# Performance work log

Measured on AMD Instinct MI355X. Metric: run time of the kernel, lower is better.

## Reference

```python
import jax, jax.numpy as jnp
import numpy as np

B, L, C, D, H, EL, DFF, NC, PH = 32, 512, 64, 512, 8, 3, 2048, 8, 256
DK = D // H


def _ln(x, g, b):
    m = jnp.mean(x, -1, keepdims=True)
    v = jnp.var(x, -1, keepdims=True)
    return (x - m) / jnp.sqrt(v + 1e-5) * g + b


def _projector(x, stats, cw, w1, b1, w2, b2, w3):
    # circular Conv1d over feature axis with seq_len input channels -> 1 channel
    xp = jnp.pad(x, ((0, 0), (0, 0), (1, 1)), mode='wrap')  # [B,L,C+2]
    win = jnp.stack([xp[:, :, :-2], xp[:, :, 1:-1], xp[:, :, 2:]], -1)  # [B,L,C,3]
    y = jnp.einsum('bsck,sk->bc', win, cw)  # [B,C]
    h = jnp.concatenate([y, stats[:, 0, :]], -1)  # [B,2C]
    h = jax.nn.relu(h @ w1.T + b1)
    h = jax.nn.relu(h @ w2.T + b2)
    return h @ w3.T


def setup_inputs() -> dict:
    key = jax.random.key(0)
    ks = jax.random.split(key, 20)
    n = lambda i, shape, s=0.02: jax.random.normal(ks[i], shape, jnp.float32) * s
    return {
        'x_enc': jax.random.normal(ks[0], (B, L, C), jnp.float32),
        'emb_conv_w': n(1, (D, C, 3), 0.05),
        'tau_conv_w': n(2, (L, 3), 0.05),
        'tau_w1': n(3, (PH, 2 * C)), 'tau_b1': jnp.zeros((PH,), jnp.float32),
        'tau_w2': n(4, (PH, PH)), 'tau_b2': jnp.zeros((PH,), jnp.float32),
        'tau_w3': n(5, (1, PH)),
        'delta_conv_w': n(6, (L, 3), 0.05),
        'delta_w1': n(7, (PH, 2 * C)), 'delta_b1': jnp.zeros((PH,), jnp.float32),
        'delta_w2': n(8, (PH, PH)), 'delta_b2': jnp.zeros((PH,), jnp.float32),
        'delta_w3': n(9, (L, PH)),
        'Wq': n(10, (EL, D, D)), 'bq': jnp.zeros((EL, D), jnp.float32),
        'Wk': n(11, (EL, D, D)), 'bk': jnp.zeros((EL, D), jnp.float32),
        'Wv': n(12, (EL, D, D)), 'bv': jnp.zeros((EL, D), jnp.float32),
        'Wo': n(13, (EL, D, D)), 'bo': jnp.zeros((EL, D), jnp.float32),
        'ff_w1': n(14, (EL, DFF, D)), 'ff_b1': jnp.zeros((EL, DFF), jnp.float32),
        'ff_w2': n(15, (EL, D, DFF)), 'ff_b2': jnp.zeros((EL, D), jnp.float32),
        'ln1_g': jnp.ones((EL, D), jnp.float32), 'ln1_b': jnp.zeros((EL, D), jnp.float32),
        'ln2_g': jnp.ones((EL, D), jnp.float32), 'ln2_b': jnp.zeros((EL, D), jnp.float32),
        'norm_g': jnp.ones((D,), jnp.float32), 'norm_b': jnp.zeros((D,), jnp.float32),
        'proj_w': n(16, (NC, D * L), 0.005), 'proj_b': jnp.zeros((NC,), jnp.float32),
    }


def reference(x_enc, emb_conv_w, tau_conv_w, tau_w1, tau_b1, tau_w2, tau_b2, tau_w3,
              delta_conv_w, delta_w1, delta_b1, delta_w2, delta_b2, delta_w3,
              Wq, bq, Wk, bk, Wv, bv, Wo, bo, ff_w1, ff_b1, ff_w2, ff_b2,
              ln1_g, ln1_b, ln2_g, ln2_b, norm_g, norm_b, proj_w, proj_b):
    x_raw = jax.lax.stop_gradient(x_enc)
    mean_enc = jax.lax.stop_gradient(jnp.mean(x_enc, 1, keepdims=True))  # [B,1,C]
    std_enc = jax.lax.stop_gradient(jnp.sqrt(jnp.var(x_enc, axis=1, keepdims=True) + 1e-5))
    tau = jnp.exp(_projector(x_raw, std_enc, tau_conv_w, tau_w1, tau_b1, tau_w2, tau_b2, tau_w3))  # [B,1]
    delta = _projector(x_raw, mean_enc, delta_conv_w, delta_w1, delta_b1, delta_w2, delta_b2, delta_w3)  # [B,L]

    # TokenEmbedding: circular Conv1d (kernel 3, no bias) over time + sinusoidal PE
    xp = jnp.pad(x_enc, ((0, 0), (1, 1), (0, 0)), mode='wrap')
    win = jnp.stack([xp[:, :-2], xp[:, 1:-1], xp[:, 2:]], -1)  # [B,L,C,3]
    x = jnp.einsum('blck,dck->bld', win, emb_conv_w)
    pos = jnp.arange(L, dtype=jnp.float32)[:, None]
    div = jnp.exp(jnp.arange(0, D, 2, dtype=jnp.float32) * (-jnp.log(10000.0) / D))
    pe = jnp.zeros((L, D), jnp.float32).at[:, 0::2].set(jnp.sin(pos * div)).at[:, 1::2].set(jnp.cos(pos * div))
    x = x + pe[None]

    scale = 1.0 / jnp.sqrt(jnp.float32(DK))
    tau4 = tau[:, :, None, None]      # [B,1,1,1]
    delta4 = delta[:, None, None, :]  # [B,1,1,S]
    for i in range(EL):
        q = (x @ Wq[i].T + bq[i]).reshape(B, L, H, DK)
        k = (x @ Wk[i].T + bk[i]).reshape(B, L, H, DK)
        v = (x @ Wv[i].T + bv[i]).reshape(B, L, H, DK)
        scores = jnp.einsum('blhe,bshe->bhls', q, k) * tau4 + delta4  # DSAttention rescale/shift
        A = jax.nn.softmax(scale * scores, axis=-1)
        o = jnp.einsum('bhls,bshd->blhd', A, v).reshape(B, L, D)
        x = x + (o @ Wo[i].T + bo[i])
        x = _ln(x, ln1_g[i], ln1_b[i])
        y = jax.nn.gelu(x @ ff_w1[i].T + ff_b1[i], approximate=False)  # conv1 kernel=1 == linear
        y = y @ ff_w2[i].T + ff_b2[i]
        x = _ln(x + y, ln2_g[i], ln2_b[i])
    x = _ln(x, norm_g, norm_b)
    out = jax.nn.gelu(x, approximate=False).reshape(B, -1)
    return out @ proj_w.T + proj_b
```

## Files before the change

### kernel.cpp

```cpp
#include <hip/hip_runtime.h>
#include <hip/hip_bf16.h>
#include <math.h>

#define B_   32
#define L_   512
#define C_   64
#define D_   512
#define H_   8
#define EL_  3
#define DFF_ 2048
#define NC_  8
#define PH_  256
#define DK_  64
#define NTOK (B_*L_)

typedef unsigned short u16;
typedef unsigned int   u32;
typedef __attribute__((ext_vector_type(4))) float f32x4;
typedef __attribute__((ext_vector_type(8))) short s16x8;

__device__ __forceinline__ u16 f2b(float f){
  u32 u = __float_as_uint(f);
  u32 r = (u + 0x7fffu + ((u >> 16) & 1u)) >> 16;
  return (u16)r;
}
__device__ __forceinline__ float b2f(u16 u){ return __uint_as_float(((u32)u) << 16); }

__device__ __forceinline__ void gload16(const void* g, void* l){
  __builtin_amdgcn_global_load_lds(
      (const __attribute__((address_space(1))) u32*)g,
      (__attribute__((address_space(3))) u32*)l, 16, 0, 0);
}

__device__ __forceinline__ float gelu_exact(float x){
  return 0.5f * x * (1.f + erff(x * 0.70710678118654752f));
}


__global__ __launch_bounds__(256) void k_stats(const float* __restrict__ x,
    float* __restrict__ mean, float* __restrict__ stdv){
  int b = blockIdx.x, t = threadIdx.x;
  const float* p = x + (size_t)b*L_*C_;
  float s = 0.f, q = 0.f;
  for (int i = t; i < L_*C_; i += 256){ float v = p[i]; s += v; q += v*v; }
  __shared__ float ss[256], qq[256];
  ss[t] = s; qq[t] = q;
  __syncthreads();
  if (t < 64){
    float S = ss[t]+ss[t+64]+ss[t+128]+ss[t+192];
    float Q = qq[t]+qq[t+64]+qq[t+128]+qq[t+192];
    float m = S*(1.f/L_);
    mean[b*64+t] = m;
    stdv[b*64+t] = sqrtf(Q*(1.f/L_) - m*m + 1e-5f);
  }
}

__global__ __launch_bounds__(256) void k_mlp(const float* __restrict__ x,
    const float* __restrict__ mean, const float* __restrict__ stdv,
    const float* __restrict__ cw_t, const float* __restrict__ w1t, const float* __restrict__ b1t,
    const float* __restrict__ w2t, const float* __restrict__ b2t, const float* __restrict__ w3t,
    const float* __restrict__ cw_d, const float* __restrict__ w1d, const float* __restrict__ b1d,
    const float* __restrict__ w2d, const float* __restrict__ b2d, const float* __restrict__ w3d,
    float* __restrict__ tau, float* __restrict__ delta)
{
  int b = blockIdx.x, sel = blockIdx.y, t = threadIdx.x;
  const float* cw = sel ? cw_d : cw_t;
  const float* w1 = sel ? w1d : w1t;  const float* b1 = sel ? b1d : b1t;
  const float* w2 = sel ? w2d : w2t;  const float* b2 = sel ? b2d : b2t;
  const float* st = sel ? mean : stdv;
  __shared__ float h0[128], h1s[256], h2s[256], red[256];
  __shared__ float c4[4][64];
  {
    int c = t & 63, g = t >> 6;
    int cm = (c+63)&63, cp = (c+1)&63;
    const float* xrow = x + (size_t)b*L_*C_;
    float acc = 0.f;
    for (int s = g*128; s < (g+1)*128; ++s){
      const float* r = xrow + s*C_;
      acc += r[cm]*cw[s*3] + r[c]*cw[s*3+1] + r[cp]*cw[s*3+2];
    }
    c4[g][c] = acc;
  }
  __syncthreads();
  if (t < 64)       h0[t] = c4[0][t]+c4[1][t]+c4[2][t]+c4[3][t];
  else if (t < 128) h0[t] = st[b*64 + (t-64)];
  __syncthreads();
  { float a = b1[t]; for (int j=0;j<128;++j) a += h0[j]*w1[t*128+j]; h1s[t] = fmaxf(a,0.f); }
  __syncthreads();
  { float a = b2[t]; for (int j=0;j<256;++j) a += h1s[j]*w2[t*256+j]; h2s[t] = fmaxf(a,0.f); }
  __syncthreads();
  if (sel == 0){
    red[t] = h2s[t]*w3t[t];
    __syncthreads();
    for (int o=128;o>0;o>>=1){ if (t<o) red[t]+=red[t+o]; __syncthreads(); }
    if (t == 0) tau[b] = expf(red[0]);
  } else {
    for (int l = t; l < L_; l += 256){
      float a = 0.f;
      for (int j=0;j<256;++j) a += h2s[j]*w3d[l*256+j];
      delta[b*L_ + l] = a;
    }
  }
}

__global__ void k_pe(float* __restrict__ pe){
  int i = blockIdx.x*256 + threadIdx.x;
  if (i >= L_*D_/2) return;
  int l = i >> 8, j = i & 255;
  float div = expf((float)(2*j) * (-9.210340371976184f / (float)D_));
  float arg = (float)l * div;
  pe[l*D_ + 2*j]   = sinf(arg);
  pe[l*D_ + 2*j+1] = cosf(arg);
}

__global__ void k_awin(const float* __restrict__ x, u16* __restrict__ awin){
  int i = blockIdx.x*256 + threadIdx.x;
  if (i >= NTOK*192) return;
  int col = i % 192, row = i / 192;
  int k = col >> 6, c = col & 63;
  int b = row >> 9, l = row & 511;
  int ls = (l + k + 511) & 511;
  awin[i] = f2b(x[((size_t)((b<<9) | ls))*64 + c]);
}

__global__ void k_embw(const float* __restrict__ w, u16* __restrict__ o){
  int i = blockIdx.x*256 + threadIdx.x;
  if (i >= D_*192) return;
  int d = i / 192, col = i % 192, k = col >> 6, c = col & 63;
  o[i] = f2b(w[(d*64 + c)*3 + k]);
}

__global__ void k_packqkv(const float* __restrict__ Wq, const float* __restrict__ Wk,
                          const float* __restrict__ Wv, u16* __restrict__ o){
  int i = blockIdx.x*256 + threadIdx.x;
  if (i >= EL_*1536*D_) return;
  int e = i / (1536*D_), r = i % (1536*D_);
  int n = r / D_, k = r % D_;
  const float* src = (n < 512) ? Wq + ((size_t)e*512 + n)*512 + k
                   : (n < 1024) ? Wk + ((size_t)e*512 + (n-512))*512 + k
                                : Wv + ((size_t)e*512 + (n-1024))*512 + k;
  o[i] = f2b(*src);
}
__global__ void k_packb(const float* __restrict__ bq, const float* __restrict__ bk,
                        const float* __restrict__ bv, float* __restrict__ o){
  int i = blockIdx.x*256 + threadIdx.x;
  if (i >= EL_*1536) return;
  int e = i/1536, n = i%1536;
  o[i] = (n<512) ? bq[e*512+n] : (n<1024) ? bk[e*512+n-512] : bv[e*512+n-1024];
}

__global__ void k_f2b(const float* __restrict__ in, u16* __restrict__ out, int n){
  int i = blockIdx.x*256 + threadIdx.x;
  if (i < n) out[i] = f2b(in[i]);
}

__global__ __launch_bounds__(256,2) void k_gemm(
    const u16* __restrict__ A, const u16* __restrict__ Bm,
    int M, int N, int K,
    const float* __restrict__ bias,
    const float* __restrict__ pe,
    int dogelu,
    float* __restrict__ outF, u16* __restrict__ outB)
{
  __shared__ u16 As[128*64];
  __shared__ u16 Bs[128*64];
  int tid = threadIdx.x;
  int l = tid & 63, w = tid >> 6;
  int wr = w >> 1, wc = w & 1;
  int lo = l & 15, lg = l >> 4;

  int flat = blockIdx.x + gridDim.x*blockIdx.y;
  int nwg  = gridDim.x*gridDim.y;
  int n1   = ((nwg & 7) == 0) ? ((flat & 7)*(nwg >> 3) + (flat >> 3)) : flat;
  int bx   = n1 % gridDim.x, by = n1 / gridDim.x;
  int m0 = by * 128, n0 = bx * 128;

  f32x4 acc[4][4];
  #pragma unroll
  for (int m=0;m<4;++m)
    #pragma unroll
    for (int n=0;n<4;++n) acc[m][n] = (f32x4){0.f,0.f,0.f,0.f};

  int ktn = K >> 6;
  for (int kt = 0; kt < ktn; ++kt){
    #pragma unroll
    for (int i=0;i<4;++i){
      int cA = i*256 + tid;
      int row = cA >> 3, colb = (cA & 7)*8;
      gload16(A  + (size_t)(m0+row)*K + kt*64 + colb, &As[cA*8]);
      gload16(Bm + (size_t)(n0+row)*K + kt*64 + colb, &Bs[cA*8]);
    }
    __syncthreads();
    #pragma unroll
    for (int kk=0;kk<2;++kk){
      int ka = kk*32 + lg*8;
      s16x8 af[4], bfr[4];
      #pragma unroll
      for (int m=0;m<4;++m) af[m]  = *(const s16x8*)&As[(wr*64 + m*16 + lo)*64 + ka];
      #pragma unroll
      for (int n=0;n<4;++n) bfr[n] = *(const s16x8*)&Bs[(wc*64 + n*16 + lo)*64 + ka];
      #pragma unroll
      for (int m=0;m<4;++m)
        #pragma unroll
        for (int n=0;n<4;++n)
          acc[m][n] = __builtin_amdgcn_mfma_f32_16x16x32_bf16(af[m], bfr[n], acc[m][n], 0,0,0);
    }
    __syncthreads();
  }

  #pragma unroll
  for (int m=0;m<4;++m){
    int rbase = m0 + wr*64 + m*16 + lg*4;
    #pragma unroll
    for (int n=0;n<4;++n){
      int col = n0 + wc*64 + n*16 + lo;
      float bv = bias ? bias[col] : 0.f;
      #pragma unroll
      for (int r=0;r<4;++r){
        int row = rbase + r;
        float v = acc[m][n][r] + bv;
        if (pe) v += pe[(size_t)(row & 511)*N + col];
        if (dogelu) v = gelu_exact(v);
        size_t o = (size_t)row*N + col;
        if (outF) outF[o] = v;
        if (outB) outB[o] = f2b(v);
      }
    }
  }
}

__global__ __launch_bounds__(256) void k_vt(const u16* __restrict__ qkv, u16* __restrict__ vT){
  int st = blockIdx.x, h = blockIdx.y, b = blockIdx.z;
  __shared__ u16 tile[64][72];
  int t = threadIdx.x;
  int r = t >> 2, q = t & 3;
  const u16* src = qkv + ((size_t)(b*L_ + st*64 + r))*1536 + 1024 + h*64 + q*16;
  #pragma unroll
  for (int j=0;j<16;++j) tile[r][q*16+j] = src[j];
  __syncthreads();
  u16* dst = vT + (((size_t)(b*H_ + h))*64 + r)*L_ + st*64 + q*16;
  #pragma unroll
  for (int j=0;j<16;++j) dst[j] = tile[q*16+j][r];
}

__global__ __launch_bounds__(256) void k_attn(
    const u16* __restrict__ qkv, const u16* __restrict__ vT,
    const float* __restrict__ tau, const float* __restrict__ delta,
    u16* __restrict__ obf)
{
  __shared__ u16 Ks[2][64*64];
  __shared__ u16 Vs[2][64*64];
  __shared__ u16 plds[4][16*64];
  int id = blockIdx.x;
  int qt = id >> 8, hb = id & 255, h = hb >> 5, b = hb & 31;
  int tid = threadIdx.x, l = tid & 63, w = tid >> 6;
  int lo = l & 15, lg = l >> 4;
  int q0 = qt*64 + w*16;

  const u16* qrow = qkv + ((size_t)(b*L_ + q0 + lo))*1536 + h*64;
  s16x8 qf0 = *(const s16x8*)(qrow + lg*8);
  s16x8 qf1 = *(const s16x8*)(qrow + 32 + lg*8);

  const u16* Kg = qkv + (size_t)b*L_*1536 + 512 + h*64;
  const u16* Vg = vT + ((size_t)(b*H_ + h))*64*L_;

  float taus = tau[b] * 0.125f;
  f32x4 oacc[4];
  #pragma unroll
  for (int n=0;n<4;++n) oacc[n] = (f32x4){0.f,0.f,0.f,0.f};
  float mrow[4] = {-3e38f,-3e38f,-3e38f,-3e38f};
  float lrow[4] = {0.f,0.f,0.f,0.f};
  const float* dptr = delta + b*L_;
  u16* pw = &plds[w][0];

  auto STAGE = [&](int buf, int s0){
    #pragma unroll
    for (int i=0;i<2;++i){
      int c = i*256 + tid;
      int row = c >> 3, sub = (c & 7) ^ (row & 7);
      gload16(Kg + (size_t)(s0 + row)*1536 + sub*8, &Ks[buf][c*8]);
      gload16(Vg + (size_t)row*L_ + s0 + sub*8,     &Vs[buf][c*8]);
    }
  };

  STAGE(0, 0);
  __syncthreads();

  int swz = lo & 7;
  for (int it = 0; it < 8; ++it){
    int s0 = it*64, cur = it & 1;
    if (it < 7) STAGE(cur^1, s0 + 64);
    const u16* Kc = &Ks[cur][0];
    const u16* Vc = &Vs[cur][0];

    f32x4 sacc[4];
    #pragma unroll
    for (int t2=0;t2<4;++t2) sacc[t2] = (f32x4){0.f,0.f,0.f,0.f};
    #pragma unroll
    for (int kk=0;kk<2;++kk){
      #pragma unroll
      for (int t2=0;t2<4;++t2){
        s16x8 kf = *(const s16x8*)&Kc[(t2*16 + lo)*64 + (((kk*4 + lg) ^ swz)*8)];
        sacc[t2] = __builtin_amdgcn_mfma_f32_16x16x32_bf16(kk ? qf1 : qf0, kf, sacc[t2], 0,0,0);
      }
    }

    float p[4][4];
    float rm[4] = {-3e38f,-3e38f,-3e38f,-3e38f};
    #pragma unroll
    for (int t2=0;t2<4;++t2){
      float dl = dptr[s0 + t2*16 + lo] * 0.125f;
      #pragma unroll
      for (int r=0;r<4;++r){
        float sc = taus*sacc[t2][r] + dl;
        p[t2][r] = sc;
        rm[r] = fmaxf(rm[r], sc);
      }
    }
    #pragma unroll
    for (int r=0;r<4;++r){
      #pragma unroll
      for (int off=1; off<16; off<<=1) rm[r] = fmaxf(rm[r], __shfl_xor(rm[r], off));
    }
    float alpha[4];
    #pragma unroll
    for (int r=0;r<4;++r){
      float mn = fmaxf(mrow[r], rm[r]);
      alpha[r] = __expf(mrow[r] - mn);
      mrow[r] = mn;
      float acc = 0.f;
      #pragma unroll
      for (int t2=0;t2<4;++t2){ p[t2][r] = __expf(p[t2][r] - mn); acc += p[t2][r]; }
      #pragma unroll
      for (int off=1; off<16; off<<=1) acc += __shfl_xor(acc, off);
      lrow[r] = lrow[r]*alpha[r] + acc;
    }
    #pragma unroll
    for (int n=0;n<4;++n)
      #pragma unroll
      for (int r=0;r<4;++r) oacc[n][r] *= alpha[r];

    #pragma unroll
    for (int t2=0;t2<4;++t2)
      #pragma unroll
      for (int r=0;r<4;++r){
        int q = lg*4 + r;
        int cb = (t2*2 + (lo>>3)) ^ (q & 7);
        pw[q*64 + cb*8 + (lo & 7)] = f2b(p[t2][r]);
      }
    asm volatile("" ::: "memory");
    #pragma unroll
    for (int kk=0;kk<2;++kk){
      s16x8 pa = *(const s16x8*)&pw[lo*64 + (((kk*4 + lg) ^ swz)*8)];
      #pragma unroll
      for (int n=0;n<4;++n){
        s16x8 vf = *(const s16x8*)&Vc[(n*16 + lo)*64 + (((kk*4 + lg) ^ swz)*8)];
        oacc[n] = __builtin_amdgcn_mfma_f32_16x16x32_bf16(pa, vf, oacc[n], 0,0,0);
      }
    }
    __syncthreads();
  }

  float inv[4];
  #pragma unroll
  for (int r=0;r<4;++r) inv[r] = 1.f / lrow[r];
  #pragma unroll
  for (int n=0;n<4;++n)
    #pragma unroll
    for (int r=0;r<4;++r){
      int row = q0 + lg*4 + r;
      int col = h*64 + n*16 + lo;
      obf[((size_t)(b*L_ + row))*512 + col] = f2b(oacc[n][r]*inv[r]);
    }
}

__global__ __launch_bounds__(256) void k_ln(const float* __restrict__ X, const float* __restrict__ R,
    const float* __restrict__ gw, const float* __restrict__ bw,
    float* __restrict__ outF, u16* __restrict__ outB, int dogelu)
{
  int l = threadIdx.x & 63, w = threadIdx.x >> 6;
  size_t row = (size_t)blockIdx.x*4 + w;
  const float4* x4 = (const float4*)(X + row*D_);
  float4 a0 = x4[l*2], a1 = x4[l*2+1];
  if (R){
    const float4* r4 = (const float4*)(R + row*D_);
    float4 c0 = r4[l*2], c1 = r4[l*2+1];
    a0.x+=c0.x; a0.y+=c0.y; a0.z+=c0.z; a0.w+=c0.w;
    a1.x+=c1.x; a1.y+=c1.y; a1.z+=c1.z; a1.w+=c1.w;
  }
  float v[8] = {a0.x,a0.y,a0.z,a0.w,a1.x,a1.y,a1.z,a1.w};
  float s = 0.f, q = 0.f;
  #pragma unroll
  for (int j=0;j<8;++j){ s += v[j]; q += v[j]*v[j]; }
  #pragma unroll
  for (int off=1; off<64; off<<=1){ s += __shfl_xor(s, off); q += __shfl_xor(q, off); }
  float mean = s * (1.f/D_);
  float var  = q * (1.f/D_) - mean*mean;
  float rstd = rsqrtf(var + 1e-5f);
  int c0i = l*8;
  #pragma unroll
  for (int j=0;j<8;++j){
    int c = c0i + j;
    float t = (v[j] - mean)*rstd*gw[c] + bw[c];
    if (dogelu) t = gelu_exact(t);
    if (outF) outF[row*D_ + c] = t;
    if (outB) outB[row*D_ + c] = f2b(t);
  }
}

__global__ __launch_bounds__(256) void k_proj1(const float* __restrict__ g, const float* __restrict__ pw,
    float* __restrict__ pp)
{
  int b = blockIdx.x, nc = blockIdx.y, kc = blockIdx.z, t = threadIdx.x;
  const float4* g4 = (const float4*)(g  + (size_t)b*(L_*D_) + (size_t)kc*32768);
  const float4* w4 = (const float4*)(pw + (size_t)nc*(L_*D_) + (size_t)kc*32768);
  float acc = 0.f;
  for (int k = t; k < 8192; k += 256){
    float4 a = g4[k], c = w4[k];
    acc += a.x*c.x + a.y*c.y + a.z*c.z + a.w*c.w;
  }
  #pragma unroll
  for (int off=1; off<64; off<<=1) acc += __shfl_xor(acc, off);
  __shared__ float red[4];
  if ((t & 63) == 0) red[t>>6] = acc;
  __syncthreads();
  if (t == 0) pp[((b*NC_ + nc)<<3) + kc] = red[0]+red[1]+red[2]+red[3];
}
__global__ void k_proj2(const float* __restrict__ pp, const float* __restrict__ pb,
                        float* __restrict__ out){
  int t = threadIdx.x;
  float s = 0.f;
  #pragma unroll
  for (int k=0;k<8;++k) s += pp[t*8 + k];
  out[t] = s + pb[t & 7];
}

extern "C" void kernel_launch(void* const* d_in, const int* in_sizes, int n_in,
                              void* d_out, int out_size, void* d_ws, size_t ws_size,
                              hipStream_t stream)
{
  const float* x_enc        = (const float*)d_in[0];
  const float* emb_conv_w   = (const float*)d_in[1];
  const float* tau_conv_w   = (const float*)d_in[2];
  const float* tau_w1       = (const float*)d_in[3];
  const float* tau_b1       = (const float*)d_in[4];
  const float* tau_w2       = (const float*)d_in[5];
  const float* tau_b2       = (const float*)d_in[6];
  const float* tau_w3       = (const float*)d_in[7];
  const float* delta_conv_w = (const float*)d_in[8];
  const float* delta_w1     = (const float*)d_in[9];
  const float* delta_b1     = (const float*)d_in[10];
  const float* delta_w2     = (const float*)d_in[11];
  const float* delta_b2     = (const float*)d_in[12];
  const float* delta_w3     = (const float*)d_in[13];
  const float* Wq  = (const float*)d_in[14];
  const float* bq  = (const float*)d_in[15];
  const float* Wk  = (const float*)d_in[16];
  const float* bk  = (const float*)d_in[17];
  const float* Wv  = (const float*)d_in[18];
  const float* bv  = (const float*)d_in[19];
  const float* Wo  = (const float*)d_in[20];
  const float* bo  = (const float*)d_in[21];
  const float* ff_w1 = (const float*)d_in[22];
  const float* ff_b1 = (const float*)d_in[23];
  const float* ff_w2 = (const float*)d_in[24];
  const float* ff_b2 = (const float*)d_in[25];
  const float* ln1_g = (const float*)d_in[26];
  const float* ln1_b = (const float*)d_in[27];
  const float* ln2_g = (const float*)d_in[28];
  const float* ln2_b = (const float*)d_in[29];
  const float* norm_g = (const float*)d_in[30];
  const float* norm_b = (const float*)d_in[31];
  const float* proj_w = (const float*)d_in[32];
  const float* proj_b = (const float*)d_in[33];
  (void)in_sizes; (void)n_in; (void)out_size; (void)ws_size;

  char* ws = (char*)d_ws;
  size_t off = 0;
  auto alloc = [&](size_t n){ size_t o = off; off += (n + 255) & ~(size_t)255; return o; };
  float* xf    = (float*)(ws + alloc((size_t)NTOK*512*4));
  u16*   xb    = (u16*)  (ws + alloc((size_t)NTOK*512*2));
  char*  U     =          ws + alloc((size_t)NTOK*2048*2);
  u16*   qkv   = (u16*)U;
  u16*   h1    = (u16*)U;
  u16*   awin  = (u16*)U;
  u16*   obf   = (u16*)(U + (size_t)NTOK*1536*2);
  u16*   vT    = (u16*)  (ws + alloc((size_t)NTOK*512*2));
  float* tmp   = (float*)(ws + alloc((size_t)NTOK*512*4));
  float* pe    = (float*)(ws + alloc((size_t)512*512*4));
  u16*   WqkvB = (u16*)  (ws + alloc((size_t)EL_*1536*512*2));
  u16*   WoB   = (u16*)  (ws + alloc((size_t)EL_*512*512*2));
  u16*   W1B   = (u16*)  (ws + alloc((size_t)EL_*2048*512*2));
  u16*   W2B   = (u16*)  (ws + alloc((size_t)EL_*512*2048*2));
  u16*   embB  = (u16*)  (ws + alloc((size_t)512*192*2));
  float* bqkv  = (float*)(ws + alloc((size_t)EL_*1536*4));
  float* meanb = (float*)(ws + alloc(2048*4));
  float* stdb  = (float*)(ws + alloc(2048*4));
  float* taub  = (float*)(ws + alloc(256));
  float* deltab= (float*)(ws + alloc((size_t)B_*512*4));
  float* pp    = (float*)(ws + alloc((size_t)B_*NC_*8*4));

  k_packqkv<<<(EL_*1536*512+255)/256, 256, 0, stream>>>(Wq, Wk, Wv, WqkvB);
  k_packb  <<<(EL_*1536+255)/256,     256, 0, stream>>>(bq, bk, bv, bqkv);
  k_f2b    <<<(EL_*512*512+255)/256,  256, 0, stream>>>(Wo, WoB, EL_*512*512);
  k_f2b    <<<(EL_*2048*512+255)/256, 256, 0, stream>>>(ff_w1, W1B, EL_*2048*512);
  k_f2b    <<<(EL_*512*2048+255)/256, 256, 0, stream>>>(ff_w2, W2B, EL_*512*2048);
  k_embw   <<<(D_*192+255)/256,       256, 0, stream>>>(emb_conv_w, embB);

  k_stats<<<B_, 256, 0, stream>>>(x_enc, meanb, stdb);
  k_mlp<<<dim3(B_,2), 256, 0, stream>>>(x_enc, meanb, stdb,
      tau_conv_w, tau_w1, tau_b1, tau_w2, tau_b2, tau_w3,
      delta_conv_w, delta_w1, delta_b1, delta_w2, delta_b2, delta_w3,
      taub, deltab);
  k_pe  <<<(L_*D_/2+255)/256, 256, 0, stream>>>(pe);
  k_awin<<<(NTOK*192+255)/256, 256, 0, stream>>>(x_enc, awin);

  k_gemm<<<dim3(4,128), 256, 0, stream>>>(awin, embB, NTOK, 512, 192, nullptr, pe, 0, xf, xb);

  for (int e = 0; e < EL_; ++e){
    k_gemm<<<dim3(12,128), 256, 0, stream>>>(xb, WqkvB + (size_t)e*1536*512, NTOK, 1536, 512,
                                             bqkv + e*1536, nullptr, 0, nullptr, qkv);
    k_vt  <<<dim3(8,8,32), 256, 0, stream>>>(qkv, vT);
    k_attn<<<2048, 256, 0, stream>>>(qkv, vT, taub, deltab, obf);
    k_gemm<<<dim3(4,128), 256, 0, stream>>>(obf, WoB + (size_t)e*512*512, NTOK, 512, 512,
                                            bo + e*512, nullptr, 0, tmp, nullptr);
    k_ln  <<<NTOK/4, 256, 0, stream>>>(xf, tmp, ln1_g + e*512, ln1_b + e*512, xf, xb, 0);
    k_gemm<<<dim3(16,128), 256, 0, stream>>>(xb, W1B + (size_t)e*2048*512, NTOK, 2048, 512,
                                             ff_b1 + e*2048, nullptr, 1, nullptr, h1);
    k_gemm<<<dim3(4,128), 256, 0, stream>>>(h1, W2B + (size_t)e*512*2048, NTOK, 512, 2048,
                                            ff_b2 + e*512, nullptr, 0, tmp, nullptr);
    k_ln  <<<NTOK/4, 256, 0, stream>>>(xf, tmp, ln2_g + e*512, ln2_b + e*512, xf,
                                       (e == EL_-1) ? nullptr : xb, 0);
  }

  k_ln   <<<NTOK/4, 256, 0, stream>>>(xf, nullptr, norm_g, norm_b, tmp, nullptr, 1);
  k_proj1<<<dim3(B_,NC_,8), 256, 0, stream>>>(tmp, proj_w, pp);
  k_proj2<<<1, 256, 0, stream>>>(pp, proj_b, (float*)d_out);
}
```

Before: 1.452 ms.

## Add double-buffered 256x256 GEMM for QKV and FFN1, swizzle LDS layout

Adds an XOR swizzle to the LDS tile layout in the existing 128x128 GEMM so that MFMA fragment reads avoid bank conflicts. Introduces a new 512-thread GEMM kernel with 256x256 tiles, double-buffered LDS staging that prefetches the next K-tile while computing the current one, and setprio hints around the MFMA bursts. The QKV and FFN1 projections now use it to get more reuse per global load and overlap loads with compute. The larger tile uses 128 KB of LDS and many accumulator registers per thread, which can lower occupancy, and the grid becomes small relative to the number of CUs.

Measured after the change: 1.496 ms. 1.03x slower.

```diff
diff --git a/kernel.cpp b/kernel.cpp
--- a/kernel.cpp
+++ b/kernel.cpp
@@ -157,8 +157,7 @@
 __global__ __launch_bounds__(256,2) void k_gemm(
     const u16* __restrict__ A, const u16* __restrict__ Bm,
     int M, int N, int K,
-    const float* __restrict__ bias,
-    const float* __restrict__ pe,
+    const float* __restrict__ bias, const float* __restrict__ pe,
     int dogelu,
     float* __restrict__ outF, u16* __restrict__ outB)
 {
@@ -181,24 +180,25 @@
     #pragma unroll
     for (int n=0;n<4;++n) acc[m][n] = (f32x4){0.f,0.f,0.f,0.f};
 
+  int swz = lo & 7;
   int ktn = K >> 6;
   for (int kt = 0; kt < ktn; ++kt){
     #pragma unroll
     for (int i=0;i<4;++i){
       int cA = i*256 + tid;
-      int row = cA >> 3, colb = (cA & 7)*8;
-      gload16(A  + (size_t)(m0+row)*K + kt*64 + colb, &As[cA*8]);
-      gload16(Bm + (size_t)(n0+row)*K + kt*64 + colb, &Bs[cA*8]);
+      int row = cA >> 3, sub = (cA & 7) ^ (row & 7);
+      gload16(A  + (size_t)(m0+row)*K + kt*64 + sub*8, &As[cA*8]);
+      gload16(Bm + (size_t)(n0+row)*K + kt*64 + sub*8, &Bs[cA*8]);
     }
     __syncthreads();
     #pragma unroll
     for (int kk=0;kk<2;++kk){
-      int ka = kk*32 + lg*8;
+      int cb = ((kk<<2)|lg) ^ swz;
       s16x8 af[4], bfr[4];
       #pragma unroll
-      for (int m=0;m<4;++m) af[m]  = *(const s16x8*)&As[(wr*64 + m*16 + lo)*64 + ka];
-      #pragma unroll
-      for (int n=0;n<4;++n) bfr[n] = *(const s16x8*)&Bs[(wc*64 + n*16 + lo)*64 + ka];
+      for (int m=0;m<4;++m) af[m]  = *(const s16x8*)&As[(wr*64 + m*16 + lo)*64 + cb*8];
+      #pragma unroll
+      for (int n=0;n<4;++n) bfr[n] = *(const s16x8*)&Bs[(wc*64 + n*16 + lo)*64 + cb*8];
       #pragma unroll
       for (int m=0;m<4;++m)
         #pragma unroll
@@ -220,6 +220,108 @@
         int row = rbase + r;
         float v = acc[m][n][r] + bv;
         if (pe) v += pe[(size_t)(row & 511)*N + col];
+        if (dogelu) v = gelu_exact(v);
+        size_t o = (size_t)row*N + col;
+        if (outF) outF[o] = v;
+        if (outB) outB[o] = f2b(v);
+      }
+    }
+  }
+}
+
+__global__ __launch_bounds__(512,2) void k_gemm256(
+    const u16* __restrict__ A, const u16* __restrict__ Bm,
+    int M, int N, int K,
+    const float* __restrict__ bias,
+    int dogelu,
+    float* __restrict__ outF, u16* __restrict__ outB)
+{
+  __shared__ u16 AS[2][256*64];
+  __shared__ u16 BS[2][256*64];
+  int tid = threadIdx.x;
+  int l = tid & 63, w = tid >> 6;
+  int wr = w >> 2, wc = w & 3;
+  int lo = l & 15, lg = l >> 4;
+  int swz = lo & 7;
+
+  int flat = blockIdx.x + gridDim.x*blockIdx.y;
+  int nwg  = gridDim.x*gridDim.y;
+  int n1   = ((nwg & 7) == 0) ? ((flat & 7)*(nwg >> 3) + (flat >> 3)) : flat;
+  int bx   = n1 % gridDim.x, by = n1 / gridDim.x;
+  int m0 = by * 256, n0 = bx * 256;
+
+  f32x4 acc[8][4];
+  #pragma unroll
+  for (int m=0;m<8;++m)
+    #pragma unroll
+    for (int n=0;n<4;++n) acc[m][n] = (f32x4){0.f,0.f,0.f,0.f};
+
+  auto STAGE = [&](int buf, int kt){
+    #pragma unroll
+    for (int i=0;i<4;++i){
+      int c = i*512 + tid;
+      int row = c >> 3, sub = (c & 7) ^ (row & 7);
+      gload16(A  + (size_t)(m0+row)*K + kt*64 + sub*8, &AS[buf][c*8]);
+      gload16(Bm + (size_t)(n0+row)*K + kt*64 + sub*8, &BS[buf][c*8]);
+    }
+  };
+
+  STAGE(0, 0);
+  __syncthreads();
+
+  int ktn = K >> 6;
+  for (int kt = 0; kt < ktn; ++kt){
+    int cur = kt & 1;
+    if (kt + 1 < ktn) STAGE(cur^1, kt+1);
+    const u16* Ac = &AS[cur][0];
+    const u16* Bc = &BS[cur][0];
+
+    #pragma unroll
+    for (int q=0;q<4;++q){
+      int qm = q >> 1, qn = q & 1;
+      s16x8 af[4][2], bf2[2][2];
+      #pragma unroll
+      for (int mm=0;mm<4;++mm)
+        #pragma unroll
+        for (int ks=0;ks<2;++ks){
+          int row = wr*128 + (qm*4+mm)*16 + lo;
+          int cb  = ((ks<<2)|lg) ^ swz;
+          af[mm][ks] = *(const s16x8*)&Ac[row*64 + cb*8];
+        }
+      #pragma unroll
+      for (int nn=0;nn<2;++nn)
+        #pragma unroll
+        for (int ks=0;ks<2;++ks){
+          int row = wc*64 + (qn*2+nn)*16 + lo;
+          int cb  = ((ks<<2)|lg) ^ swz;
+          bf2[nn][ks] = *(const s16x8*)&Bc[row*64 + cb*8];
+        }
+      __builtin_amdgcn_s_setprio(1);
+      #pragma unroll
+      for (int mm=0;mm<4;++mm)
+        #pragma unroll
+        for (int nn=0;nn<2;++nn)
+          #pragma unroll
+          for (int ks=0;ks<2;++ks)
+            acc[qm*4+mm][qn*2+nn] = __builtin_amdgcn_mfma_f32_16x16x32_bf16(
+                af[mm][ks], bf2[nn][ks], acc[qm*4+mm][qn*2+nn], 0,0,0);
+      __builtin_amdgcn_s_setprio(0);
+      __builtin_amdgcn_sched_barrier(0);
+    }
+    __syncthreads();
+  }
+
+  #pragma unroll
+  for (int m=0;m<8;++m){
+    int rbase = m0 + wr*128 + m*16 + lg*4;
+    #pragma unroll
+    for (int n=0;n<4;++n){
+      int col = n0 + wc*64 + n*16 + lo;
+      float bv = bias ? bias[col] : 0.f;
+      #pragma unroll
+      for (int r=0;r<4;++r){
+        int row = rbase + r;
+        float v = acc[m][n][r] + bv;
         if (dogelu) v = gelu_exact(v);
         size_t o = (size_t)row*N + col;
         if (outF) outF[o] = v;
@@ -518,15 +620,15 @@
   k_gemm<<<dim3(4,128), 256, 0, stream>>>(awin, embB, NTOK, 512, 192, nullptr, pe, 0, xf, xb);
 
   for (int e = 0; e < EL_; ++e){
-    k_gemm<<<dim3(12,128), 256, 0, stream>>>(xb, WqkvB + (size_t)e*1536*512, NTOK, 1536, 512,
-                                             bqkv + e*1536, nullptr, 0, nullptr, qkv);
+    k_gemm256<<<dim3(6,64), 512, 0, stream>>>(xb, WqkvB + (size_t)e*1536*512, NTOK, 1536, 512,
+                                              bqkv + e*1536, 0, nullptr, qkv);
     k_vt  <<<dim3(8,8,32), 256, 0, stream>>>(qkv, vT);
     k_attn<<<2048, 256, 0, stream>>>(qkv, vT, taub, deltab, obf);
     k_gemm<<<dim3(4,128), 256, 0, stream>>>(obf, WoB + (size_t)e*512*512, NTOK, 512, 512,
                                             bo + e*512, nullptr, 0, tmp, nullptr);
     k_ln  <<<NTOK/4, 256, 0, stream>>>(xf, tmp, ln1_g + e*512, ln1_b + e*512, xf, xb, 0);
-    k_gemm<<<dim3(16,128), 256, 0, stream>>>(xb, W1B + (size_t)e*2048*512, NTOK, 2048, 512,
-                                             ff_b1 + e*2048, nullptr, 1, nullptr, h1);
+    k_gemm256<<<dim3(8,64), 512, 0, stream>>>(xb, W1B + (size_t)e*2048*512, NTOK, 2048, 512,
+                                              ff_b1 + e*2048, 1, nullptr, h1);
     k_gemm<<<dim3(4,128), 256, 0, stream>>>(h1, W2B + (size_t)e*512*2048, NTOK, 512, 2048,
                                             ff_b2 + e*512, nullptr, 0, tmp, nullptr);
     k_ln  <<<NTOK/4, 256, 0, stream>>>(xf, tmp, ln2_g + e*512, ln2_b + e*512, xf,
```
